# Performance work log

Hardware: AMD Instinct MI355X
Metric: run time of the kernel (lower is better)

Reference implementation:

```python
import jax, jax.numpy as jnp
import numpy as np

IN_CH = 128
OUT_CH = 128
N_NODES = 50000
N_EDGES = 800000
BN_EPS = 1e-5


def setup_inputs() -> dict:
    key = jax.random.key(0)
    k_x, k_e, k_wl, k_bl, k_wr = jax.random.split(key, 5)
    x = jax.random.normal(k_x, (N_NODES, IN_CH), dtype=jnp.float32)
    edge_index = jax.random.randint(k_e, (2, N_EDGES), 0, N_NODES, dtype=jnp.int64)
    s = 1.0 / np.sqrt(IN_CH)
    W_l = jax.random.uniform(k_wl, (OUT_CH, IN_CH), jnp.float32, -s, s)  # lin_l: aggregated neighbors
    b_l = jax.random.uniform(k_bl, (OUT_CH,), jnp.float32, -s, s)
    W_r = jax.random.uniform(k_wr, (OUT_CH, IN_CH), jnp.float32, -s, s)  # lin_r: root/self
    gamma = jnp.ones((OUT_CH,), jnp.float32)
    beta = jnp.zeros((OUT_CH,), jnp.float32)
    return {"x": x, "edge_index": edge_index, "W_l": W_l, "b_l": b_l,
            "W_r": W_r, "gamma": gamma, "beta": beta}


def reference(x, edge_index, W_l, b_l, W_r, gamma, beta):
    n = x.shape[0]
    src, dst = edge_index[0], edge_index[1]
    # gather source features and mean-aggregate at destination nodes
    msgs = x[src]                                              # [E, C_in]
    agg = jax.ops.segment_sum(msgs, dst, num_segments=n)      # [N, C_in]
    deg = jax.ops.segment_sum(jnp.ones((edge_index.shape[1],), x.dtype), dst, num_segments=n)
    mean_agg = agg / jnp.maximum(deg, 1.0)[:, None]
    # SAGEConv: lin_l(aggregated) + lin_r(self)
    h = mean_agg @ W_l.T + b_l + x @ W_r.T                     # [N, C_out]
    # BatchNorm1d (training-mode batch statistics, biased variance)
    mu = h.mean(axis=0)
    var = ((h - mu) ** 2).mean(axis=0)
    h = (h - mu) * jax.lax.rsqrt(var + BN_EPS) * gamma + beta
    return jax.nn.relu(h)
```

## Files before the change

kernel.cpp:

```cpp
#include <hip/hip_runtime.h>

#define CH 128
#define BN_EPS 1e-5f

typedef unsigned int uint32;
typedef unsigned short ushort16;
using f32x4  = __attribute__((ext_vector_type(4))) float;
using bf16x8 = __attribute__((ext_vector_type(8))) short;

__device__ __forceinline__ ushort16 f2b(float f) {
    uint32 u = __float_as_uint(f);
    return (ushort16)((u + 0x7FFFu + ((u >> 16) & 1u)) >> 16);
}

__global__ __launch_bounds__(256) void sage_prep(
    const float* __restrict__ x, const void* __restrict__ ei,
    const float* __restrict__ Wl, const float* __restrict__ Wr,
    int* __restrict__ head, int2* __restrict__ pair,
    uint32* __restrict__ xb4, uint2* __restrict__ xq8,
    ushort16* __restrict__ wct, float* __restrict__ bn,
    int nEdges, int total8)
{
    const int* pi = (const int*)ei;
    int lane = threadIdx.x & 63;
    int probe = pi[lane * 2 + 1];
    bool is64 = (__ballot(probe != 0) == 0ULL);

    int e = blockIdx.x * 256 + threadIdx.x;
    if (e < nEdges) {
        int s, d;
        if (is64) {
            const long long* p = (const long long*)ei;
            s = (int)p[e];
            d = (int)p[nEdges + e];
        } else {
            s = pi[e];
            d = pi[nEdges + e];
        }
        int old = atomicExch(&head[d], e);
        pair[e] = make_int2(old, s);
    }

    int i = blockIdx.x * 256 + threadIdx.x;
    if (i < total8) {
        const float4* x4 = (const float4*)x;
        float4 a = x4[2 * i], b = x4[2 * i + 1];
        uint4 o;
        o.x = (uint32)f2b(a.x) | ((uint32)f2b(a.y) << 16);
        o.y = (uint32)f2b(a.z) | ((uint32)f2b(a.w) << 16);
        o.z = (uint32)f2b(b.x) | ((uint32)f2b(b.y) << 16);
        o.w = (uint32)f2b(b.z) | ((uint32)f2b(b.w) << 16);
        ((uint4*)xb4)[i] = o;

        int qa = __builtin_amdgcn_cvt_pk_fp8_f32(a.x, a.y, 0, false);
        qa = __builtin_amdgcn_cvt_pk_fp8_f32(a.z, a.w, qa, true);
        int qb = __builtin_amdgcn_cvt_pk_fp8_f32(b.x, b.y, 0, false);
        qb = __builtin_amdgcn_cvt_pk_fp8_f32(b.z, b.w, qb, true);
        xq8[i] = make_uint2((uint32)qa, (uint32)qb);
    }

    if (blockIdx.x < 128) {
        int idx = blockIdx.x * 256 + threadIdx.x;
        int co = idx >> 8, k = idx & 255;
        float v = (k < 128) ? Wr[co * 128 + k] : Wl[co * 128 + (k - 128)];
        wct[idx] = f2b(v);
    }
    if (blockIdx.x == 0) bn[threadIdx.x] = 0.f;
    if (blockIdx.x == 1 && threadIdx.x < 32)
        ((uint32*)(xq8))[(size_t)total8 * 2 + threadIdx.x] = 0;
}

__global__ __launch_bounds__(256) void sage_aggregate(
    const char* __restrict__ xq, const int* __restrict__ head,
    const int2* __restrict__ pair, uint32* __restrict__ mean_b, int nNodes)
{
    int wid = blockIdx.x * 4 + (threadIdx.x >> 6);
    int nbase = wid * 4;
    if (nbase >= nNodes) return;
    int lane = threadIdx.x & 63;
    int half = lane >> 5;
    int sub = lane & 31;

    const int ZROW = nNodes;

    int cur = -1;
    if (lane < 4) {
        int n = nbase + lane;
        cur = (n < nNodes) ? head[n] : -1;
    }
    int cnt = 0;
    float4 accA = {0.f, 0.f, 0.f, 0.f};
    float4 accB = {0.f, 0.f, 0.f, 0.f};

    while (__ballot(cur >= 0) != 0ULL) {
        int2 pr = make_int2(-1, ZROW);
        if (cur >= 0) pr = pair[cur];
        int s0 = __shfl(pr.y, 0), s1 = __shfl(pr.y, 1);
        int s2 = __shfl(pr.y, 2), s3 = __shfl(pr.y, 3);

        int sA = half ? s1 : s0;
        int sB = half ? s3 : s2;
        uint32 uA = *(const uint32*)(xq + ((size_t)sA << 7) + sub * 4);
        uint32 uB = *(const uint32*)(xq + ((size_t)sB << 7) + sub * 4);

        accA.x += __builtin_amdgcn_cvt_f32_fp8(uA, 0);
        accA.y += __builtin_amdgcn_cvt_f32_fp8(uA, 1);
        accA.z += __builtin_amdgcn_cvt_f32_fp8(uA, 2);
        accA.w += __builtin_amdgcn_cvt_f32_fp8(uA, 3);
        accB.x += __builtin_amdgcn_cvt_f32_fp8(uB, 0);
        accB.y += __builtin_amdgcn_cvt_f32_fp8(uB, 1);
        accB.z += __builtin_amdgcn_cvt_f32_fp8(uB, 2);
        accB.w += __builtin_amdgcn_cvt_f32_fp8(uB, 3);

        if (cur >= 0) { ++cnt; cur = pr.x; }
    }

    int cA = __shfl(cnt, half);
    int cB = __shfl(cnt, 2 + half);
    float invA = 1.0f / fmaxf((float)cA, 1.0f);
    float invB = 1.0f / fmaxf((float)cB, 1.0f);

    int nA = nbase + half;
    if (nA < nNodes) {
        uint2 o;
        o.x = (uint32)f2b(accA.x * invA) | ((uint32)f2b(accA.y * invA) << 16);
        o.y = (uint32)f2b(accA.z * invA) | ((uint32)f2b(accA.w * invA) << 16);
        *(uint2*)((char*)mean_b + (size_t)nA * 256 + sub * 8) = o;
    }
    int nB = nbase + 2 + half;
    if (nB < nNodes) {
        uint2 o;
        o.x = (uint32)f2b(accB.x * invB) | ((uint32)f2b(accB.y * invB) << 16);
        o.y = (uint32)f2b(accB.z * invB) | ((uint32)f2b(accB.w * invB) << 16);
        *(uint2*)((char*)mean_b + (size_t)nB * 256 + sub * 8) = o;
    }
}

__global__ __launch_bounds__(256) void sage_gemm(
    const ushort16* __restrict__ xb, const ushort16* __restrict__ mean_b,
    const ushort16* __restrict__ wct, const float* __restrict__ bl,
    float* __restrict__ h, float* __restrict__ bn, int nNodes)
{
    __shared__ ushort16 wsh[8 * 8 * 64 * 8];
    __shared__ float redS[4][CH];
    __shared__ float redQ[4][CH];

    int tid = threadIdx.x;
    int wave = tid >> 6, lane = tid & 63;
    int col = lane & 15, kg = lane >> 4;

    #pragma unroll
    for (int it = 0; it < 16; ++it) {
        int pidx = wave * 16 + it;
        int cb = pidx >> 3, ks = pidx & 7;
        bf16x8 v = *(const bf16x8*)(wct + (size_t)(cb * 16 + col) * 256 + ks * 32 + kg * 8);
        *(bf16x8*)(wsh + ((size_t)pidx * 64 + lane) * 8) = v;
    }

    int rowBase = blockIdx.x * 64 + wave * 16;
    int arow = min(rowBase + col, nNodes - 1);
    const ushort16* xrow = xb + (size_t)arow * CH;
    const ushort16* mrow = mean_b + (size_t)arow * CH;

    bf16x8 afrag[8];
    #pragma unroll
    for (int t = 0; t < 4; ++t)
        afrag[t] = *(const bf16x8*)(xrow + t * 32 + kg * 8);
    #pragma unroll
    for (int t = 0; t < 4; ++t)
        afrag[4 + t] = *(const bf16x8*)(mrow + t * 32 + kg * 8);

    __syncthreads();

    f32x4 acc[8];
    #pragma unroll
    for (int cb = 0; cb < 8; ++cb) acc[cb] = (f32x4){0.f, 0.f, 0.f, 0.f};

    #pragma unroll
    for (int kstep = 0; kstep < 8; ++kstep) {
        bf16x8 a = afrag[kstep];
        #pragma unroll
        for (int cb = 0; cb < 8; ++cb) {
            bf16x8 b = *(const bf16x8*)(wsh + ((size_t)(cb * 8 + kstep) * 64 + lane) * 8);
            acc[cb] = __builtin_amdgcn_mfma_f32_16x16x32_bf16(a, b, acc[cb], 0, 0, 0);
        }
    }

    #pragma unroll
    for (int cb = 0; cb < 8; ++cb) {
        int co = cb * 16 + col;
        float blv = bl[co];
        float s = 0.f, ss = 0.f;
        #pragma unroll
        for (int j = 0; j < 4; ++j) {
            int r = rowBase + kg * 4 + j;
            float v = acc[cb][j] + blv;
            if (r < nNodes) {
                h[(size_t)r * CH + co] = v;
                s += v;
                ss += v * v;
            }
        }
        s  += __shfl_xor(s, 16);  s  += __shfl_xor(s, 32);
        ss += __shfl_xor(ss, 16); ss += __shfl_xor(ss, 32);
        if (kg == 0) { redS[wave][co] = s; redQ[wave][co] = ss; }
    }
    __syncthreads();
    if (tid < CH) {
        atomicAdd(&bn[tid], redS[0][tid] + redS[1][tid] + redS[2][tid] + redS[3][tid]);
    } else {
        int c = tid - CH;
        atomicAdd(&bn[CH + c], redQ[0][c] + redQ[1][c] + redQ[2][c] + redQ[3][c]);
    }
}

__global__ __launch_bounds__(256) void sage_apply(
    float* __restrict__ h, const float* __restrict__ bn,
    const float* __restrict__ gamma, const float* __restrict__ beta,
    int total4, int nNodes)
{
    __shared__ float sc_sh[CH], sh_sh[CH];
    int tid = threadIdx.x;
    if (tid < CH) {
        float invN = 1.0f / (float)nNodes;
        float mu = bn[tid] * invN;
        float var = fmaxf(bn[CH + tid] * invN - mu * mu, 0.f);
        float sc = gamma[tid] * rsqrtf(var + BN_EPS);
        sc_sh[tid] = sc;
        sh_sh[tid] = beta[tid] - mu * sc;
    }
    __syncthreads();
    int i = blockIdx.x * 256 + tid;
    if (i >= total4) return;
    float4 v = reinterpret_cast<float4*>(h)[i];
    int c = (i * 4) & 127;
    float4 sc = *reinterpret_cast<const float4*>(&sc_sh[c]);
    float4 sh = *reinterpret_cast<const float4*>(&sh_sh[c]);
    v.x = fmaxf(fmaf(v.x, sc.x, sh.x), 0.f);
    v.y = fmaxf(fmaf(v.y, sc.y, sh.y), 0.f);
    v.z = fmaxf(fmaf(v.z, sc.z, sh.z), 0.f);
    v.w = fmaxf(fmaf(v.w, sc.w, sh.w), 0.f);
    reinterpret_cast<float4*>(h)[i] = v;
}

extern "C" void kernel_launch(void* const* d_in, const int* in_sizes, int n_in,
                              void* d_out, int out_size, void* d_ws, size_t ws_size,
                              hipStream_t stream)
{
    const float* x     = (const float*)d_in[0];
    const void*  ei    = d_in[1];
    const float* Wl    = (const float*)d_in[2];
    const float* bl    = (const float*)d_in[3];
    const float* Wr    = (const float*)d_in[4];
    const float* gamma = (const float*)d_in[5];
    const float* beta  = (const float*)d_in[6];

    int nNodes = in_sizes[0] / CH;
    int nEdges = in_sizes[1] / 2;
    int nBlkM  = (nNodes + 63) / 64;

    char* p = (char*)d_ws;
    auto take = [&](size_t bytes) {
        char* r = p;
        p += (bytes + 255) & ~(size_t)255;
        return r;
    };
    ushort16* xb      = (ushort16*)take((size_t)nNodes * CH * 2);
    char*     xq      = (char*)take((size_t)nNodes * CH + 128);
    ushort16* mean_b  = (ushort16*)take((size_t)nNodes * CH * 2);
    ushort16* wct     = (ushort16*)take((size_t)CH * 256 * 2);
    int*      head    = (int*)take((size_t)nNodes * 4);
    float*    bn      = (float*)take(256 * 4);
    int2*     pair    = (int2*)take((size_t)nEdges * 8);

    float* h = (float*)d_out;

    hipMemsetAsync(head, 0xFF, (size_t)nNodes * 4, stream);

    int total8 = nNodes * CH / 8;
    int eBlocks = (nEdges + 255) / 256;
    int pBlocks = max(eBlocks, (total8 + 255) / 256);
    sage_prep<<<pBlocks, 256, 0, stream>>>(
        x, ei, Wl, Wr, head, pair, (uint32*)xb, (uint2*)xq, wct, bn,
        nEdges, total8);

    int aBlocks = (nNodes + 15) / 16;
    sage_aggregate<<<aBlocks, 256, 0, stream>>>(
        xq, head, pair, (uint32*)mean_b, nNodes);

    sage_gemm<<<nBlkM, 256, 0, stream>>>(
        xb, mean_b, wct, bl, h, bn, nNodes);

    int total4 = nNodes * CH / 4;
    sage_apply<<<(total4 + 255) / 256, 256, 0, stream>>>(
        h, bn, gamma, beta, total4, nNodes);
}
```

Baseline: 134.2 us.

## Walk eight adjacency chains per wave with 16-byte gathers; double prep work per thread

The aggregation kernel now assigns 8 destination nodes per wavefront instead of 4. Each group of 8 lanes gathers a full 128-byte FP8 row with 16-byte loads and keeps 16 accumulators, writing the bf16 mean with 32-byte stores. This is meant to raise memory-level parallelism per wave and cut the number of gather instructions. The trade-off is that each wave loops until its longest of 8 chains finishes, so more lanes sit idle on uneven degrees, and register use rises. The prep kernel also handles two edges and two 8-element feature chunks per thread with wider stores, halving its grid.

```diff
diff --git a/kernel.cpp b/kernel.cpp
--- a/kernel.cpp
+++ b/kernel.cpp
@@ -11,6 +11,9 @@
 __device__ __forceinline__ ushort16 f2b(float f) {
     uint32 u = __float_as_uint(f);
     return (ushort16)((u + 0x7FFFu + ((u >> 16) & 1u)) >> 16);
+}
+__device__ __forceinline__ uint32 pk2(float a, float b) {
+    return (uint32)f2b(a) | ((uint32)f2b(b) << 16);
 }
 
 __global__ __launch_bounds__(256) void sage_prep(
@@ -26,44 +29,67 @@
     int probe = pi[lane * 2 + 1];
     bool is64 = (__ballot(probe != 0) == 0ULL);
 
-    int e = blockIdx.x * 256 + threadIdx.x;
-    if (e < nEdges) {
-        int s, d;
+    int idx = blockIdx.x * 256 + threadIdx.x;
+    int e0 = idx * 2, e1 = e0 + 1;
+    if (e0 < nEdges) {
+        bool has1 = (e1 < nEdges);
+        int s0, d0, s1 = 0, d1 = 0;
         if (is64) {
             const long long* p = (const long long*)ei;
-            s = (int)p[e];
-            d = (int)p[nEdges + e];
+            long long a0 = p[e0];
+            long long a1 = has1 ? p[e1] : 0;
+            long long b0 = p[nEdges + e0];
+            long long b1 = has1 ? p[nEdges + e1] : 0;
+            s0 = (int)a0; s1 = (int)a1; d0 = (int)b0; d1 = (int)b1;
         } else {
-            s = pi[e];
-            d = pi[nEdges + e];
-        }
-        int old = atomicExch(&head[d], e);
-        pair[e] = make_int2(old, s);
-    }
-
-    int i = blockIdx.x * 256 + threadIdx.x;
-    if (i < total8) {
+            s0 = pi[e0]; s1 = has1 ? pi[e1] : 0;
+            d0 = pi[nEdges + e0]; d1 = has1 ? pi[nEdges + e1] : 0;
+        }
+        int old0 = atomicExch(&head[d0], e0);
+        int old1 = has1 ? atomicExch(&head[d1], e1) : 0;
+        if (has1) {
+            int4 pk = make_int4(old0, s0, old1, s1);
+            *(int4*)(pair + e0) = pk;
+        } else {
+            pair[e0] = make_int2(old0, s0);
+        }
+    }
+
+    int i0 = idx * 2, i1 = i0 + 1;
+    if (i0 < total8) {
         const float4* x4 = (const float4*)x;
-        float4 a = x4[2 * i], b = x4[2 * i + 1];
-        uint4 o;
-        o.x = (uint32)f2b(a.x) | ((uint32)f2b(a.y) << 16);
-        o.y = (uint32)f2b(a.z) | ((uint32)f2b(a.w) << 16);
-        o.z = (uint32)f2b(b.x) | ((uint32)f2b(b.y) << 16);
-        o.w = (uint32)f2b(b.z) | ((uint32)f2b(b.w) << 16);
-        ((uint4*)xb4)[i] = o;
+        float4 a = x4[2 * i0], b = x4[2 * i0 + 1];
+        bool has1 = (i1 < total8);
+        float4 c = has1 ? x4[2 * i1] : make_float4(0, 0, 0, 0);
+        float4 d = has1 ? x4[2 * i1 + 1] : make_float4(0, 0, 0, 0);
+
+        uint4 o0 = make_uint4(pk2(a.x, a.y), pk2(a.z, a.w), pk2(b.x, b.y), pk2(b.z, b.w));
+        ((uint4*)xb4)[i0] = o0;
+        if (has1) {
+            uint4 o1 = make_uint4(pk2(c.x, c.y), pk2(c.z, c.w), pk2(d.x, d.y), pk2(d.z, d.w));
+            ((uint4*)xb4)[i1] = o1;
+        }
 
         int qa = __builtin_amdgcn_cvt_pk_fp8_f32(a.x, a.y, 0, false);
         qa = __builtin_amdgcn_cvt_pk_fp8_f32(a.z, a.w, qa, true);
         int qb = __builtin_amdgcn_cvt_pk_fp8_f32(b.x, b.y, 0, false);
         qb = __builtin_amdgcn_cvt_pk_fp8_f32(b.z, b.w, qb, true);
-        xq8[i] = make_uint2((uint32)qa, (uint32)qb);
+        if (has1) {
+            int qc = __builtin_amdgcn_cvt_pk_fp8_f32(c.x, c.y, 0, false);
+            qc = __builtin_amdgcn_cvt_pk_fp8_f32(c.z, c.w, qc, true);
+            int qd = __builtin_amdgcn_cvt_pk_fp8_f32(d.x, d.y, 0, false);
+            qd = __builtin_amdgcn_cvt_pk_fp8_f32(d.z, d.w, qd, true);
+            *(uint4*)(xq8 + i0) = make_uint4((uint32)qa, (uint32)qb, (uint32)qc, (uint32)qd);
+        } else {
+            xq8[i0] = make_uint2((uint32)qa, (uint32)qb);
+        }
     }
 
     if (blockIdx.x < 128) {
-        int idx = blockIdx.x * 256 + threadIdx.x;
-        int co = idx >> 8, k = idx & 255;
+        int widx = blockIdx.x * 256 + threadIdx.x;
+        int co = widx >> 8, k = widx & 255;
         float v = (k < 128) ? Wr[co * 128 + k] : Wl[co * 128 + (k - 128)];
-        wct[idx] = f2b(v);
+        wct[widx] = f2b(v);
     }
     if (blockIdx.x == 0) bn[threadIdx.x] = 0.f;
     if (blockIdx.x == 1 && threadIdx.x < 32)
@@ -75,64 +101,55 @@
     const int2* __restrict__ pair, uint32* __restrict__ mean_b, int nNodes)
 {
     int wid = blockIdx.x * 4 + (threadIdx.x >> 6);
-    int nbase = wid * 4;
+    int nbase = wid * 8;
     if (nbase >= nNodes) return;
     int lane = threadIdx.x & 63;
-    int half = lane >> 5;
-    int sub = lane & 31;
+    int chain = lane >> 3;
+    int sub = lane & 7;
 
     const int ZROW = nNodes;
 
     int cur = -1;
-    if (lane < 4) {
+    if (lane < 8) {
         int n = nbase + lane;
         cur = (n < nNodes) ? head[n] : -1;
     }
     int cnt = 0;
-    float4 accA = {0.f, 0.f, 0.f, 0.f};
-    float4 accB = {0.f, 0.f, 0.f, 0.f};
+    float acc[16];
+    #pragma unroll
+    for (int i = 0; i < 16; ++i) acc[i] = 0.f;
 
     while (__ballot(cur >= 0) != 0ULL) {
         int2 pr = make_int2(-1, ZROW);
         if (cur >= 0) pr = pair[cur];
-        int s0 = __shfl(pr.y, 0), s1 = __shfl(pr.y, 1);
-        int s2 = __shfl(pr.y, 2), s3 = __shfl(pr.y, 3);
-
-        int sA = half ? s1 : s0;
-        int sB = half ? s3 : s2;
-        uint32 uA = *(const uint32*)(xq + ((size_t)sA << 7) + sub * 4);
-        uint32 uB = *(const uint32*)(xq + ((size_t)sB << 7) + sub * 4);
-
-        accA.x += __builtin_amdgcn_cvt_f32_fp8(uA, 0);
-        accA.y += __builtin_amdgcn_cvt_f32_fp8(uA, 1);
-        accA.z += __builtin_amdgcn_cvt_f32_fp8(uA, 2);
-        accA.w += __builtin_amdgcn_cvt_f32_fp8(uA, 3);
-        accB.x += __builtin_amdgcn_cvt_f32_fp8(uB, 0);
-        accB.y += __builtin_amdgcn_cvt_f32_fp8(uB, 1);
-        accB.z += __builtin_amdgcn_cvt_f32_fp8(uB, 2);
-        accB.w += __builtin_amdgcn_cvt_f32_fp8(uB, 3);
-
+        int s = __shfl(pr.y, chain);
+        uint4 u = *(const uint4*)(xq + ((size_t)s << 7) + sub * 16);
+        #pragma unroll
+        for (int w = 0; w < 4; ++w) {
+            uint32 uw = (&u.x)[w];
+            acc[w * 4 + 0] += __builtin_amdgcn_cvt_f32_fp8(uw, 0);
+            acc[w * 4 + 1] += __builtin_amdgcn_cvt_f32_fp8(uw, 1);
+            acc[w * 4 + 2] += __builtin_amdgcn_cvt_f32_fp8(uw, 2);
+            acc[w * 4 + 3] += __builtin_amdgcn_cvt_f32_fp8(uw, 3);
+        }
         if (cur >= 0) { ++cnt; cur = pr.x; }
     }
 
-    int cA = __shfl(cnt, half);
-    int cB = __shfl(cnt, 2 + half);
-    float invA = 1.0f / fmaxf((float)cA, 1.0f);
-    float invB = 1.0f / fmaxf((float)cB, 1.0f);
-
-    int nA = nbase + half;
-    if (nA < nNodes) {
-        uint2 o;
-        o.x = (uint32)f2b(accA.x * invA) | ((uint32)f2b(accA.y * invA) << 16);
-        o.y = (uint32)f2b(accA.z * invA) | ((uint32)f2b(accA.w * invA) << 16);
-        *(uint2*)((char*)mean_b + (size_t)nA * 256 + sub * 8) = o;
-    }
-    int nB = nbase + 2 + half;
-    if (nB < nNodes) {
-        uint2 o;
-        o.x = (uint32)f2b(accB.x * invB) | ((uint32)f2b(accB.y * invB) << 16);
-        o.y = (uint32)f2b(accB.z * invB) | ((uint32)f2b(accB.w * invB) << 16);
-        *(uint2*)((char*)mean_b + (size_t)nB * 256 + sub * 8) = o;
+    int cn = __shfl(cnt, chain);
+    float inv = 1.0f / fmaxf((float)cn, 1.0f);
+    int n = nbase + chain;
+    if (n < nNodes) {
+        uint4 o0 = make_uint4(pk2(acc[0] * inv, acc[1] * inv),
+                              pk2(acc[2] * inv, acc[3] * inv),
+                              pk2(acc[4] * inv, acc[5] * inv),
+                              pk2(acc[6] * inv, acc[7] * inv));
+        uint4 o1 = make_uint4(pk2(acc[8] * inv, acc[9] * inv),
+                              pk2(acc[10] * inv, acc[11] * inv),
+                              pk2(acc[12] * inv, acc[13] * inv),
+                              pk2(acc[14] * inv, acc[15] * inv));
+        char* base = (char*)mean_b + (size_t)n * 256 + sub * 32;
+        *(uint4*)base = o0;
+        *(uint4*)(base + 16) = o1;
     }
 }
 
@@ -278,13 +295,14 @@
     hipMemsetAsync(head, 0xFF, (size_t)nNodes * 4, stream);
 
     int total8 = nNodes * CH / 8;
-    int eBlocks = (nEdges + 255) / 256;
-    int pBlocks = max(eBlocks, (total8 + 255) / 256);
+    int ePairs = (nEdges + 1) / 2;
+    int cPairs = (total8 + 1) / 2;
+    int pBlocks = (max(ePairs, cPairs) + 255) / 256;
     sage_prep<<<pBlocks, 256, 0, stream>>>(
         x, ei, Wl, Wr, head, pair, (uint32*)xb, (uint2*)xq, wct, bn,
         nEdges, total8);
 
-    int aBlocks = (nNodes + 15) / 16;
+    int aBlocks = (nNodes + 31) / 32;
     sage_aggregate<<<aBlocks, 256, 0, stream>>>(
         xq, head, pair, (uint32*)mean_b, nNodes);
 
```

After: 125.3 us. -6.6%, faster.
